# Kernel optimization log

Hardware: AMD Instinct MI355X
Metric: run time of the kernel (lower is better)

The kernel has to match this reference:

```python
import jax, jax.numpy as jnp
import numpy as np

B, N, D, OUT = 1024, 64, 512, 2048


def setup_inputs() -> dict:
    key = jax.random.key(0)
    k1, k2, k3, k4 = jax.random.split(key, 4)
    semantic_vec = jax.random.normal(k1, (B, D), dtype=jnp.float32)
    vertices = jax.random.normal(k2, (N, D), dtype=jnp.float32)
    # per-branch Linear weights/biases, stacked: W[n] is [OUT, D], b[n] is [OUT]
    scale = 1.0 / np.sqrt(D)
    W = jax.random.uniform(k3, (N, OUT, D), dtype=jnp.float32, minval=-scale, maxval=scale)
    b = jax.random.uniform(k4, (N, OUT), dtype=jnp.float32, minval=-scale, maxval=scale)
    return {"semantic_vec": semantic_vec, "vertices": vertices, "W": W, "b": b}


def reference(semantic_vec, vertices, W, b):
    # offsets: [B, N, D] = semantic_vec broadcast-minus each vertice
    offsets = semantic_vec[:, None, :] - vertices[None, :, :]
    # per-branch linear: [B, N, OUT]
    resp = jnp.einsum('bnd,nod->bno', offsets, W) + b[None, :, :]
    resp = jax.nn.relu(resp)
    # sum over the N branches -> [B, OUT]
    return resp.sum(axis=1)
```

## Files before the change

### kernel.cpp

```cpp
#include <hip/hip_runtime.h>
#include <hip/hip_bf16.h>


typedef __attribute__((ext_vector_type(8))) short  bf16x8;
typedef __attribute__((ext_vector_type(4))) short  bf16x4;
typedef __attribute__((ext_vector_type(4))) float  f32x4;

constexpr int B   = 1024;
constexpr int N   = 64;
constexpr int D   = 512;
constexpr int OUT = 2048;

constexpr int BM  = 128;
constexpr int BO  = 64;
constexpr int TPB = 512;

static __device__ __forceinline__ unsigned short f2bf(float f) {
    unsigned int u = __builtin_bit_cast(unsigned int, f);
    u += 0x7FFFu + ((u >> 16) & 1u);
    return (unsigned short)(u >> 16);
}

static __device__ __forceinline__ bf16x4 cvt4(float4 a) {
    bf16x4 r;
    r[0] = (short)f2bf(a.x); r[1] = (short)f2bf(a.y);
    r[2] = (short)f2bf(a.z); r[3] = (short)f2bf(a.w);
    return r;
}

static __device__ __forceinline__ bf16x8 cvt8(float4 a, float4 b) {
    bf16x8 r;
    r[0] = (short)f2bf(a.x); r[1] = (short)f2bf(a.y);
    r[2] = (short)f2bf(a.z); r[3] = (short)f2bf(a.w);
    r[4] = (short)f2bf(b.x); r[5] = (short)f2bf(b.y);
    r[6] = (short)f2bf(b.z); r[7] = (short)f2bf(b.w);
    return r;
}

__global__ __launch_bounds__(256) void prep_kernel(const float* __restrict__ W,
                                                   const float* __restrict__ V,
                                                   const float* __restrict__ bias,
                                                   unsigned short* __restrict__ Wb,
                                                   float* __restrict__ c) {
    const int wid  = (blockIdx.x * 256 + threadIdx.x) >> 6;
    const int lane = threadIdx.x & 63;
    const int n = wid >> 11;

    const size_t rbase = (size_t)wid * D;
    float4 w0 = *reinterpret_cast<const float4*>(W + rbase + lane * 4);
    float4 w1 = *reinterpret_cast<const float4*>(W + rbase + 256 + lane * 4);
    float4 v0 = *reinterpret_cast<const float4*>(V + (size_t)n * D + lane * 4);
    float4 v1 = *reinterpret_cast<const float4*>(V + (size_t)n * D + 256 + lane * 4);

    *reinterpret_cast<bf16x4*>(Wb + rbase + lane * 4)       = cvt4(w0);
    *reinterpret_cast<bf16x4*>(Wb + rbase + 256 + lane * 4) = cvt4(w1);

    float s = w0.x * v0.x + w0.y * v0.y + w0.z * v0.z + w0.w * v0.w
            + w1.x * v1.x + w1.y * v1.y + w1.z * v1.z + w1.w * v1.w;
    #pragma unroll
    for (int off = 1; off < 64; off <<= 1) s += __shfl_xor(s, off);
    if (lane == 0) c[wid] = bias[wid] - s;
}

__global__ __launch_bounds__(TPB) void main_kernel(const float* __restrict__ S,
                                                   const unsigned short* __restrict__ Wb,
                                                   const float* __restrict__ C,
                                                   float* __restrict__ out) {
    __shared__ unsigned short As[BM * D];

    const int t    = threadIdx.x;
    const int lane = t & 63;
    const int w    = t >> 6;
    const int og   = w & 3;
    const int ng   = w >> 2;
    const int l15  = lane & 15;
    const int lg   = lane >> 4;
    const int ob0  = blockIdx.x * BO;
    const int bm0  = blockIdx.y * BM;
    const int ocol = ob0 + og * 16 + l15;

    #pragma unroll
    for (int i = 0; i < (BM * D / 8) / TPB; ++i) {
        int cid = i * TPB + t;
        int row = cid >> 6;
        int kc  = cid & 63;
        const float4* sp = reinterpret_cast<const float4*>(S + (size_t)(bm0 + row) * D + kc * 8);
        bf16x8 val = cvt8(sp[0], sp[1]);
        *reinterpret_cast<bf16x8*>(&As[row * D + ((kc ^ (row & 7)) * 8)]) = val;
    }
    __syncthreads();

    f32x4 oacc[8];
    #pragma unroll
    for (int mi = 0; mi < 8; ++mi) oacc[mi] = (f32x4){0.f, 0.f, 0.f, 0.f};

    const int kofs = lg * 8;

    for (int nc = 0; nc < 8; ++nc) {
        const int n0 = ng * 32 + nc * 4;

        f32x4 pre[4][8];
        #pragma unroll
        for (int j = 0; j < 4; ++j)
            #pragma unroll
            for (int mi = 0; mi < 8; ++mi) pre[j][mi] = (f32x4){0.f, 0.f, 0.f, 0.f};

        const unsigned short* wbase = Wb + ((size_t)n0 * OUT + ocol) * D + kofs;

        #pragma unroll 2
        for (int ks = 0; ks < 16; ++ks) {
            bf16x8 bq[4];
            #pragma unroll
            for (int j = 0; j < 4; ++j)
                bq[j] = *reinterpret_cast<const bf16x8*>(wbase + (size_t)j * (OUT * D) + ks * 32);

            const int kc = ks * 4 + lg;
            #pragma unroll
            for (int mi = 0; mi < 8; ++mi) {
                const int row = mi * 16 + l15;
                bf16x8 aq = *reinterpret_cast<const bf16x8*>(
                    &As[row * D + ((kc ^ (row & 7)) * 8)]);
                pre[0][mi] = __builtin_amdgcn_mfma_f32_16x16x32_bf16(aq, bq[0], pre[0][mi], 0, 0, 0);
                pre[1][mi] = __builtin_amdgcn_mfma_f32_16x16x32_bf16(aq, bq[1], pre[1][mi], 0, 0, 0);
                pre[2][mi] = __builtin_amdgcn_mfma_f32_16x16x32_bf16(aq, bq[2], pre[2][mi], 0, 0, 0);
                pre[3][mi] = __builtin_amdgcn_mfma_f32_16x16x32_bf16(aq, bq[3], pre[3][mi], 0, 0, 0);
            }
        }

        #pragma unroll
        for (int j = 0; j < 4; ++j) {
            const float cv = C[(n0 + j) * OUT + ocol];
            #pragma unroll
            for (int mi = 0; mi < 8; ++mi)
                #pragma unroll
                for (int r = 0; r < 4; ++r)
                    oacc[mi][r] += fmaxf(pre[j][mi][r] + cv, 0.f);
        }
    }

    __syncthreads();
    float* red = reinterpret_cast<float*>(As);
    if (ng == 1) {
        #pragma unroll
        for (int mi = 0; mi < 8; ++mi)
            *reinterpret_cast<f32x4*>(&red[(og * 64 + lane) * 32 + mi * 4]) = oacc[mi];
    }
    __syncthreads();
    if (ng == 0) {
        #pragma unroll
        for (int mi = 0; mi < 8; ++mi) {
            f32x4 o2 = *reinterpret_cast<const f32x4*>(&red[(og * 64 + lane) * 32 + mi * 4]);
            #pragma unroll
            for (int r = 0; r < 4; ++r) {
                int row = bm0 + mi * 16 + lg * 4 + r;
                out[(size_t)row * OUT + ocol] = oacc[mi][r] + o2[r];
            }
        }
    }
}

__global__ __launch_bounds__(TPB) void fused_kernel(const float* __restrict__ S,
                                                    const float* __restrict__ W,
                                                    const float* __restrict__ V,
                                                    const float* __restrict__ bias,
                                                    float* __restrict__ out) {
    __shared__ unsigned short As[BM * D];

    const int t    = threadIdx.x;
    const int lane = t & 63;
    const int w    = t >> 6;
    const int og   = w & 3;
    const int ng   = w >> 2;
    const int l15  = lane & 15;
    const int lg   = lane >> 4;
    const int ob0  = blockIdx.x * BO;
    const int bm0  = blockIdx.y * BM;
    const int ocol = ob0 + og * 16 + l15;

    #pragma unroll
    for (int i = 0; i < (BM * D / 8) / TPB; ++i) {
        int cid = i * TPB + t;
        int row = cid >> 6;
        int kc  = cid & 63;
        const float4* sp = reinterpret_cast<const float4*>(S + (size_t)(bm0 + row) * D + kc * 8);
        bf16x8 val = cvt8(sp[0], sp[1]);
        *reinterpret_cast<bf16x8*>(&As[row * D + ((kc ^ (row & 7)) * 8)]) = val;
    }
    __syncthreads();

    f32x4 oacc[8];
    #pragma unroll
    for (int mi = 0; mi < 8; ++mi) oacc[mi] = (f32x4){0.f, 0.f, 0.f, 0.f};

    const int kofs = lg * 8;

    for (int nc = 0; nc < 8; ++nc) {
        const int n0 = ng * 32 + nc * 4;

        f32x4 pre[4][8];
        #pragma unroll
        for (int j = 0; j < 4; ++j)
            #pragma unroll
            for (int mi = 0; mi < 8; ++mi) pre[j][mi] = (f32x4){0.f, 0.f, 0.f, 0.f};

        float cacc[4] = {0.f, 0.f, 0.f, 0.f};

        const float* wbase = W + ((size_t)n0 * OUT + ocol) * D + kofs;
        const float* vbase = V + (size_t)n0 * D + kofs;

        #pragma unroll 2
        for (int ks = 0; ks < 16; ++ks) {
            bf16x8 bq[4];
            #pragma unroll
            for (int j = 0; j < 4; ++j) {
                const float* wr = wbase + (size_t)j * (OUT * D) + ks * 32;
                float4 wa = *reinterpret_cast<const float4*>(wr);
                float4 wb = *reinterpret_cast<const float4*>(wr + 4);
                const float* vr = vbase + (size_t)j * D + ks * 32;
                float4 va = *reinterpret_cast<const float4*>(vr);
                float4 vb = *reinterpret_cast<const float4*>(vr + 4);
                cacc[j] += wa.x * va.x + wa.y * va.y + wa.z * va.z + wa.w * va.w
                         + wb.x * vb.x + wb.y * vb.y + wb.z * vb.z + wb.w * vb.w;
                bq[j] = cvt8(wa, wb);
            }
            const int kc = ks * 4 + lg;
            #pragma unroll
            for (int mi = 0; mi < 8; ++mi) {
                const int row = mi * 16 + l15;
                bf16x8 aq = *reinterpret_cast<const bf16x8*>(
                    &As[row * D + ((kc ^ (row & 7)) * 8)]);
                pre[0][mi] = __builtin_amdgcn_mfma_f32_16x16x32_bf16(aq, bq[0], pre[0][mi], 0, 0, 0);
                pre[1][mi] = __builtin_amdgcn_mfma_f32_16x16x32_bf16(aq, bq[1], pre[1][mi], 0, 0, 0);
                pre[2][mi] = __builtin_amdgcn_mfma_f32_16x16x32_bf16(aq, bq[2], pre[2][mi], 0, 0, 0);
                pre[3][mi] = __builtin_amdgcn_mfma_f32_16x16x32_bf16(aq, bq[3], pre[3][mi], 0, 0, 0);
            }
        }

        #pragma unroll
        for (int j = 0; j < 4; ++j) {
            float cs = cacc[j];
            cs += __shfl_xor(cs, 16);
            cs += __shfl_xor(cs, 32);
            const float cv = bias[(n0 + j) * OUT + ocol] - cs;
            #pragma unroll
            for (int mi = 0; mi < 8; ++mi)
                #pragma unroll
                for (int r = 0; r < 4; ++r)
                    oacc[mi][r] += fmaxf(pre[j][mi][r] + cv, 0.f);
        }
    }

    __syncthreads();
    float* red = reinterpret_cast<float*>(As);
    if (ng == 1) {
        #pragma unroll
        for (int mi = 0; mi < 8; ++mi)
            *reinterpret_cast<f32x4*>(&red[(og * 64 + lane) * 32 + mi * 4]) = oacc[mi];
    }
    __syncthreads();
    if (ng == 0) {
        #pragma unroll
        for (int mi = 0; mi < 8; ++mi) {
            f32x4 o2 = *reinterpret_cast<const f32x4*>(&red[(og * 64 + lane) * 32 + mi * 4]);
            #pragma unroll
            for (int r = 0; r < 4; ++r) {
                int row = bm0 + mi * 16 + lg * 4 + r;
                out[(size_t)row * OUT + ocol] = oacc[mi][r] + o2[r];
            }
        }
    }
}

extern "C" void kernel_launch(void* const* d_in, const int* in_sizes, int n_in,
                              void* d_out, int out_size, void* d_ws, size_t ws_size,
                              hipStream_t stream) {
    const float* S    = (const float*)d_in[0];
    const float* V    = (const float*)d_in[1];
    const float* W    = (const float*)d_in[2];
    const float* bias = (const float*)d_in[3];
    float* out = (float*)d_out;

    const size_t wb_bytes = (size_t)N * OUT * D * sizeof(unsigned short);
    const size_t c_bytes  = (size_t)N * OUT * sizeof(float);

    if (ws_size >= wb_bytes + c_bytes) {
        unsigned short* Wb = (unsigned short*)d_ws;
        float* c = (float*)((char*)d_ws + wb_bytes);
        prep_kernel<<<dim3((N * OUT) / 4), dim3(256), 0, stream>>>(W, V, bias, Wb, c);
        main_kernel<<<dim3(OUT / BO, B / BM), dim3(TPB), 0, stream>>>(S, Wb, c, out);
    } else {
        fused_kernel<<<dim3(OUT / BO, B / BM), dim3(TPB), 0, stream>>>(S, W, V, bias, out);
    }
}
```

Before: 199.3 us.

## Halve batch tile, remap block order for L2 locality, raise occupancy

Shrinks the batch tile of the main kernel from 128 to 64 rows, which halves LDS use and accumulator registers. The launch bounds now request 4 blocks per CU. The grid becomes 1-D with a custom block-to-tile mapping, so neighbouring blocks share output columns or batch rows and reuse the bf16 weights in L2 (likely spread across XCDs). The reduction scratch layout also changes to contiguous per-lane f32x4 writes, which should cut LDS bank conflicts. The trade-off is that each weight fragment is now reused across half as many rows, roughly doubling global/L2 weight traffic per unit of FLOPs. The fallback kernel is hardcoded to the old tile sizes.

Result: slower. 303.3 us (+52.2%).

```diff
diff --git a/kernel.cpp b/kernel.cpp
--- a/kernel.cpp
+++ b/kernel.cpp
@@ -11,7 +11,7 @@
 constexpr int D   = 512;
 constexpr int OUT = 2048;
 
-constexpr int BM  = 128;
+constexpr int BM  = 64;
 constexpr int BO  = 64;
 constexpr int TPB = 512;
 
@@ -62,11 +62,17 @@
     if (lane == 0) c[wid] = bias[wid] - s;
 }
 
-__global__ __launch_bounds__(TPB) void main_kernel(const float* __restrict__ S,
-                                                   const unsigned short* __restrict__ Wb,
-                                                   const float* __restrict__ C,
-                                                   float* __restrict__ out) {
+__global__ __launch_bounds__(TPB, 4) void main_kernel(const float* __restrict__ S,
+                                                      const unsigned short* __restrict__ Wb,
+                                                      const float* __restrict__ C,
+                                                      float* __restrict__ out) {
     __shared__ unsigned short As[BM * D];
+
+    const int bid   = blockIdx.x;
+    const int o_idx = (bid & 7) * 4 + (bid >> 7);
+    const int b_idx = (bid >> 3) & 15;
+    const int ob0   = o_idx * BO;
+    const int bm0   = b_idx * BM;
 
     const int t    = threadIdx.x;
     const int lane = t & 63;
@@ -75,8 +81,6 @@
     const int ng   = w >> 2;
     const int l15  = lane & 15;
     const int lg   = lane >> 4;
-    const int ob0  = blockIdx.x * BO;
-    const int bm0  = blockIdx.y * BM;
     const int ocol = ob0 + og * 16 + l15;
 
     #pragma unroll
@@ -90,20 +94,20 @@
     }
     __syncthreads();
 
-    f32x4 oacc[8];
-    #pragma unroll
-    for (int mi = 0; mi < 8; ++mi) oacc[mi] = (f32x4){0.f, 0.f, 0.f, 0.f};
+    f32x4 oacc[4];
+    #pragma unroll
+    for (int mi = 0; mi < 4; ++mi) oacc[mi] = (f32x4){0.f, 0.f, 0.f, 0.f};
 
     const int kofs = lg * 8;
 
     for (int nc = 0; nc < 8; ++nc) {
         const int n0 = ng * 32 + nc * 4;
 
-        f32x4 pre[4][8];
+        f32x4 pre[4][4];
         #pragma unroll
         for (int j = 0; j < 4; ++j)
             #pragma unroll
-            for (int mi = 0; mi < 8; ++mi) pre[j][mi] = (f32x4){0.f, 0.f, 0.f, 0.f};
+            for (int mi = 0; mi < 4; ++mi) pre[j][mi] = (f32x4){0.f, 0.f, 0.f, 0.f};
 
         const unsigned short* wbase = Wb + ((size_t)n0 * OUT + ocol) * D + kofs;
 
@@ -116,7 +120,7 @@
 
             const int kc = ks * 4 + lg;
             #pragma unroll
-            for (int mi = 0; mi < 8; ++mi) {
+            for (int mi = 0; mi < 4; ++mi) {
                 const int row = mi * 16 + l15;
                 bf16x8 aq = *reinterpret_cast<const bf16x8*>(
                     &As[row * D + ((kc ^ (row & 7)) * 8)]);
@@ -131,7 +135,7 @@
         for (int j = 0; j < 4; ++j) {
             const float cv = C[(n0 + j) * OUT + ocol];
             #pragma unroll
-            for (int mi = 0; mi < 8; ++mi)
+            for (int mi = 0; mi < 4; ++mi)
                 #pragma unroll
                 for (int r = 0; r < 4; ++r)
                     oacc[mi][r] += fmaxf(pre[j][mi][r] + cv, 0.f);
@@ -142,14 +146,14 @@
     float* red = reinterpret_cast<float*>(As);
     if (ng == 1) {
         #pragma unroll
-        for (int mi = 0; mi < 8; ++mi)
-            *reinterpret_cast<f32x4*>(&red[(og * 64 + lane) * 32 + mi * 4]) = oacc[mi];
+        for (int mi = 0; mi < 4; ++mi)
+            *reinterpret_cast<f32x4*>(&red[(og * 4 + mi) * 256 + lane * 4]) = oacc[mi];
     }
     __syncthreads();
     if (ng == 0) {
         #pragma unroll
-        for (int mi = 0; mi < 8; ++mi) {
-            f32x4 o2 = *reinterpret_cast<const f32x4*>(&red[(og * 64 + lane) * 32 + mi * 4]);
+        for (int mi = 0; mi < 4; ++mi) {
+            f32x4 o2 = *reinterpret_cast<const f32x4*>(&red[(og * 4 + mi) * 256 + lane * 4]);
             #pragma unroll
             for (int r = 0; r < 4; ++r) {
                 int row = bm0 + mi * 16 + lg * 4 + r;
@@ -159,12 +163,12 @@
     }
 }
 
-__global__ __launch_bounds__(TPB) void fused_kernel(const float* __restrict__ S,
+__global__ __launch_bounds__(512) void fused_kernel(const float* __restrict__ S,
                                                     const float* __restrict__ W,
                                                     const float* __restrict__ V,
                                                     const float* __restrict__ bias,
                                                     float* __restrict__ out) {
-    __shared__ unsigned short As[BM * D];
+    __shared__ unsigned short As[128 * D];
 
     const int t    = threadIdx.x;
     const int lane = t & 63;
@@ -173,13 +177,13 @@
     const int ng   = w >> 2;
     const int l15  = lane & 15;
     const int lg   = lane >> 4;
-    const int ob0  = blockIdx.x * BO;
-    const int bm0  = blockIdx.y * BM;
+    const int ob0  = blockIdx.x * 64;
+    const int bm0  = blockIdx.y * 128;
     const int ocol = ob0 + og * 16 + l15;
 
     #pragma unroll
-    for (int i = 0; i < (BM * D / 8) / TPB; ++i) {
-        int cid = i * TPB + t;
+    for (int i = 0; i < (128 * D / 8) / 512; ++i) {
+        int cid = i * 512 + t;
         int row = cid >> 6;
         int kc  = cid & 63;
         const float4* sp = reinterpret_cast<const float4*>(S + (size_t)(bm0 + row) * D + kc * 8);
@@ -255,13 +259,13 @@
     if (ng == 1) {
         #pragma unroll
         for (int mi = 0; mi < 8; ++mi)
-            *reinterpret_cast<f32x4*>(&red[(og * 64 + lane) * 32 + mi * 4]) = oacc[mi];
+            *reinterpret_cast<f32x4*>(&red[(og * 8 + mi) * 256 + lane * 4]) = oacc[mi];
     }
     __syncthreads();
     if (ng == 0) {
         #pragma unroll
         for (int mi = 0; mi < 8; ++mi) {
-            f32x4 o2 = *reinterpret_cast<const f32x4*>(&red[(og * 64 + lane) * 32 + mi * 4]);
+            f32x4 o2 = *reinterpret_cast<const f32x4*>(&red[(og * 8 + mi) * 256 + lane * 4]);
             #pragma unroll
             for (int r = 0; r < 4; ++r) {
                 int row = bm0 + mi * 16 + lg * 4 + r;
@@ -287,8 +291,8 @@
         unsigned short* Wb = (unsigned short*)d_ws;
         float* c = (float*)((char*)d_ws + wb_bytes);
         prep_kernel<<<dim3((N * OUT) / 4), dim3(256), 0, stream>>>(W, V, bias, Wb, c);
-        main_kernel<<<dim3(OUT / BO, B / BM), dim3(TPB), 0, stream>>>(S, Wb, c, out);
+        main_kernel<<<dim3((OUT / BO) * (B / BM)), dim3(TPB), 0, stream>>>(S, Wb, c, out);
     } else {
-        fused_kernel<<<dim3(OUT / BO, B / BM), dim3(TPB), 0, stream>>>(S, W, V, bias, out);
-    }
-}
+        fused_kernel<<<dim3(OUT / 64, B / 128), dim3(512), 0, stream>>>(S, W, V, bias, out);
+    }
+}
```
